# Optimization experiments

Measured on AMD Instinct MI355X. Metric: run time of the kernel, lower is better.

Reference implementation:

```python
import jax, jax.numpy as jnp
import numpy as np

DIM = 192
HEADS = 6
WS = 7          # window size
SHIFT = 3       # shift size
HID = 768       # mlp hidden
EPS = 1e-5


def _rel_pos_index(ws):
    coords = np.stack(np.meshgrid(np.arange(ws), np.arange(ws), indexing='ij'))  # (2, ws, ws)
    cf = coords.reshape(2, -1)                       # (2, ws*ws)
    rel = cf[:, :, None] - cf[:, None, :]            # (2, N, N)
    rel = rel.transpose(1, 2, 0).astype(np.int64)
    rel[:, :, 0] += ws - 1
    rel[:, :, 1] += ws - 1
    rel[:, :, 0] *= 2 * ws - 1
    return jnp.asarray(rel.sum(-1))                  # (N, N)

REL_IDX = _rel_pos_index(WS)


def _layernorm(x, w, b):
    mu = jnp.mean(x, axis=-1, keepdims=True)
    var = jnp.mean(jnp.square(x - mu), axis=-1, keepdims=True)
    return (x - mu) * jax.lax.rsqrt(var + EPS) * w + b


def setup_inputs() -> dict:
    key = jax.random.key(0)
    ks = jax.random.split(key, 8)
    B, H, W = 32, 56, 56
    s = 0.02
    return {
        'x': jax.random.normal(ks[0], (B, H * W, DIM), jnp.float32),
        'norm1_w': jnp.ones((DIM,), jnp.float32),
        'norm1_b': jnp.zeros((DIM,), jnp.float32),
        'qkv_w': jax.random.normal(ks[1], (3 * DIM, DIM), jnp.float32) * s,
        'qkv_b': jnp.zeros((3 * DIM,), jnp.float32),
        'rpb_table': jax.random.normal(ks[2], ((2 * WS - 1) ** 2, HEADS), jnp.float32) * s,
        'proj_w': jax.random.normal(ks[3], (DIM, DIM), jnp.float32) * s,
        'proj_b': jnp.zeros((DIM,), jnp.float32),
        'norm2_w': jnp.ones((DIM,), jnp.float32),
        'norm2_b': jnp.zeros((DIM,), jnp.float32),
        'fc1_w': jax.random.normal(ks[4], (HID, DIM), jnp.float32) * s,
        'fc1_b': jnp.zeros((HID,), jnp.float32),
        'fc2_w': jax.random.normal(ks[5], (DIM, HID), jnp.float32) * s,
        'fc2_b': jnp.zeros((DIM,), jnp.float32),
        'H': H,
        'W': W,
    }


def reference(x, norm1_w, norm1_b, qkv_w, qkv_b, rpb_table, proj_w, proj_b,
              norm2_w, norm2_b, fc1_w, fc1_b, fc2_w, fc2_b, H, W):
    B, L, C = x.shape
    d = C // HEADS
    scale = d ** -0.5
    N = WS * WS

    shortcut = x
    h = _layernorm(x, norm1_w, norm1_b).reshape(B, H, W, C)
    if SHIFT > 0:
        h = jnp.roll(h, shift=(-SHIFT, -SHIFT), axis=(1, 2))

    # window partition -> (B * nW, N, C)
    h = h.reshape(B, H // WS, WS, W // WS, WS, C).transpose(0, 1, 3, 2, 4, 5)
    hw = h.reshape(-1, N, C)

    # windowed attention (NOTE: the torch block never passes a shift mask)
    qkv = hw @ qkv_w.T + qkv_b                                    # (B_, N, 3C)
    qkv = qkv.reshape(-1, N, 3, HEADS, d).transpose(2, 0, 3, 1, 4)
    q, k, v = qkv[0] * scale, qkv[1], qkv[2]                      # (B_, h, N, d)
    attn = jnp.einsum('bhnd,bhmd->bhnm', q, k)
    bias = rpb_table[REL_IDX].transpose(2, 0, 1)                  # (h, N, N)
    attn = jax.nn.softmax(attn + bias[None], axis=-1)
    out = jnp.einsum('bhnm,bhmd->bhnd', attn, v)
    out = out.transpose(0, 2, 1, 3).reshape(-1, N, C)
    out = out @ proj_w.T + proj_b

    # window reverse -> (B, H, W, C)
    out = out.reshape(B, H // WS, W // WS, WS, WS, C).transpose(0, 1, 3, 2, 4, 5)
    out = out.reshape(B, H, W, C)
    if SHIFT > 0:
        out = jnp.roll(out, shift=(SHIFT, SHIFT), axis=(1, 2))

    x = shortcut + out.reshape(B, L, C)
    h2 = _layernorm(x, norm2_w, norm2_b)
    mlp = jax.nn.gelu(h2 @ fc1_w.T + fc1_b, approximate=False) @ fc2_w.T + fc2_b
    return x + mlp
```

## Files before the change

kernel.cpp:

```cpp
#include <hip/hip_runtime.h>
#include <hip/hip_bf16.h>
#include <cmath>

typedef float f32x4 __attribute__((ext_vector_type(4)));
typedef __bf16 bf16x8 __attribute__((ext_vector_type(8)));

#define WS_SZ 7
#define SHIFT 3
#define HGRID 56
#define C_DIM 192
#define NHEADS 6
#define HDIM 32
#define NTOK 100352
#define NWIN 2048

__device__ __forceinline__ int win_to_tok(int wrow) {
    int w = wrow / 49, i = wrow - w * 49;
    int b = w >> 6, rem = w & 63;
    int wy = rem >> 3, wx = rem & 7;
    int yi = i / 7, xi = i - yi * 7;
    int y = wy * 7 + yi + SHIFT; if (y >= HGRID) y -= HGRID;
    int x = wx * 7 + xi + SHIFT; if (x >= HGRID) x -= HGRID;
    return b * (HGRID * HGRID) + y * HGRID + x;
}

__global__ __launch_bounds__(256)
void cvt_kernel(const float* __restrict__ src, __bf16* __restrict__ dst, int n8)
{
    int idx = blockIdx.x * 256 + threadIdx.x;
    if (idx >= n8) return;
    float4 a = ((const float4*)src)[idx * 2];
    float4 b = ((const float4*)src)[idx * 2 + 1];
    bf16x8 o;
    o[0] = (__bf16)a.x; o[1] = (__bf16)a.y; o[2] = (__bf16)a.z; o[3] = (__bf16)a.w;
    o[4] = (__bf16)b.x; o[5] = (__bf16)b.y; o[6] = (__bf16)b.z; o[7] = (__bf16)b.w;
    ((bf16x8*)dst)[idx] = o;
}

__global__ __launch_bounds__(256)
void bias_expand_kernel(const float* __restrict__ rpb, float* __restrict__ bias_g)
{
    int idx = blockIdx.x * 256 + threadIdx.x;
    if (idx >= NHEADS * 2401) return;
    int h = idx / 2401, rem = idx - h * 2401;
    int i = rem / 49, j = rem - i * 49;
    int yi = i / 7, xi = i - yi * 7;
    int yj = j / 7, xj = j - yj * 7;
    int ri = (yi - yj + 6) * 13 + (xi - xj + 6);
    bias_g[idx] = rpb[ri * NHEADS + h];
}

template<int WINDOWED>
__global__ __launch_bounds__(256)
void ln_kernel(const float* __restrict__ x, const float* __restrict__ w,
               const float* __restrict__ b, __bf16* __restrict__ out)
{
    int r = blockIdx.x * 4 + (threadIdx.x >> 6);
    int lane = threadIdx.x & 63;
    int src = WINDOWED ? win_to_tok(r) : r;
    const float* xp = x + (size_t)src * C_DIM;
    float v0 = xp[lane], v1 = xp[lane + 64], v2 = xp[lane + 128];
    float s = v0 + v1 + v2;
    float sq = v0 * v0 + v1 * v1 + v2 * v2;
    #pragma unroll
    for (int off = 32; off; off >>= 1) {
        s  += __shfl_xor(s, off);
        sq += __shfl_xor(sq, off);
    }
    float mu = s * (1.f / C_DIM);
    float rs = rsqrtf(sq * (1.f / C_DIM) - mu * mu + 1e-5f);
    __bf16* op = out + (size_t)r * C_DIM;
    op[lane]       = (__bf16)((v0 - mu) * rs * w[lane]       + b[lane]);
    op[lane + 64]  = (__bf16)((v1 - mu) * rs * w[lane + 64]  + b[lane + 64]);
    op[lane + 128] = (__bf16)((v2 - mu) * rs * w[lane + 128] + b[lane + 128]);
}

template<int MODE>
__global__ __launch_bounds__(256)
void gemm_kernel(const __bf16* __restrict__ A, const __bf16* __restrict__ W,
                 const float* __restrict__ bias, void* __restrict__ outp,
                 const float* __restrict__ resid, int N, int K)
{
    __shared__ __bf16 As[128 * 40];
    __shared__ __bf16 Bs[64 * 40];
    const int tid = threadIdx.x;
    const int wave = tid >> 6, lane = tid & 63;
    const int wm = wave >> 1, wn = wave & 1;
    const int l15 = lane & 15, q8 = (lane >> 4) << 3;
    const int m0 = blockIdx.y * 128, n0 = blockIdx.x * 64;

    f32x4 acc[4][2];
    f32x4 zero = {0.f, 0.f, 0.f, 0.f};
    #pragma unroll
    for (int i = 0; i < 4; i++)
        #pragma unroll
        for (int j = 0; j < 2; j++) acc[i][j] = zero;

    const int br = tid >> 2, bc = (tid & 3) << 3;
    for (int kt = 0; kt < K; kt += 32) {
        __syncthreads();
        #pragma unroll
        for (int it = 0; it < 2; it++) {
            int idx = it * 256 + tid;
            int r = idx >> 2, c = (idx & 3) << 3;
            *(uint4*)(&As[r * 40 + c]) =
                *(const uint4*)(A + (size_t)(m0 + r) * K + kt + c);
        }
        *(uint4*)(&Bs[br * 40 + bc]) =
            *(const uint4*)(W + (size_t)(n0 + br) * K + kt + bc);
        __syncthreads();
        bf16x8 af[4], bfr[2];
        #pragma unroll
        for (int fm = 0; fm < 4; fm++)
            af[fm] = *(const bf16x8*)(&As[(wm * 64 + fm * 16 + l15) * 40 + q8]);
        #pragma unroll
        for (int fn = 0; fn < 2; fn++)
            bfr[fn] = *(const bf16x8*)(&Bs[(wn * 32 + fn * 16 + l15) * 40 + q8]);
        #pragma unroll
        for (int fm = 0; fm < 4; fm++)
            #pragma unroll
            for (int fn = 0; fn < 2; fn++)
                acc[fm][fn] = __builtin_amdgcn_mfma_f32_16x16x32_bf16(
                    af[fm], bfr[fn], acc[fm][fn], 0, 0, 0);
    }

    const int l4 = lane >> 4;
    #pragma unroll
    for (int fm = 0; fm < 4; fm++) {
        #pragma unroll
        for (int fn = 0; fn < 2; fn++) {
            int c = n0 + wn * 32 + fn * 16 + l15;
            float bv = bias[c];
            #pragma unroll
            for (int r = 0; r < 4; r++) {
                int m = m0 + wm * 64 + fm * 16 + l4 * 4 + r;
                float v = acc[fm][fn][r] + bv;
                if (MODE == 0) {
                    ((__bf16*)outp)[(size_t)m * N + c] = (__bf16)v;
                } else {
                    int t = win_to_tok(m);
                    ((float*)outp)[(size_t)t * C_DIM + c] =
                        resid[(size_t)t * C_DIM + c] + v;
                }
            }
        }
    }
}

__global__ __launch_bounds__(256, 3)
void mlp_fused_kernel(const float* __restrict__ n2w, const float* __restrict__ n2b,
                      const __bf16* __restrict__ w1,
                      const float* __restrict__ b1,
                      const __bf16* __restrict__ w2,
                      const float* __restrict__ b2,
                      float* __restrict__ out)
{
    __shared__ __bf16 As[64 * 200];
    __shared__ __bf16 Hs[64 * 136];
    const int tid = threadIdx.x;
    const int wn = tid >> 6, lane = tid & 63;
    const int l15 = lane & 15, q4 = lane >> 4, q8 = q4 << 3;
    const int m0 = blockIdx.x * 64;

    {
        const float wl0 = n2w[lane], wl1 = n2w[lane + 64], wl2 = n2w[lane + 128];
        const float bl0 = n2b[lane], bl1 = n2b[lane + 64], bl2 = n2b[lane + 128];
        const int r0 = wn * 16;
        for (int rr = 0; rr < 16; ++rr) {
            int r = r0 + rr;
            const float* xp = out + (size_t)(m0 + r) * C_DIM;
            float v0 = xp[lane], v1 = xp[lane + 64], v2 = xp[lane + 128];
            float s = v0 + v1 + v2;
            float sq = v0 * v0 + v1 * v1 + v2 * v2;
            #pragma unroll
            for (int off = 32; off; off >>= 1) {
                s  += __shfl_xor(s, off);
                sq += __shfl_xor(sq, off);
            }
            float mu = s * (1.f / C_DIM);
            float rs = rsqrtf(sq * (1.f / C_DIM) - mu * mu + 1e-5f);
            As[r * 200 + lane]       = (__bf16)((v0 - mu) * rs * wl0 + bl0);
            As[r * 200 + lane + 64]  = (__bf16)((v1 - mu) * rs * wl1 + bl1);
            As[r * 200 + lane + 128] = (__bf16)((v2 - mu) * rs * wl2 + bl2);
        }
    }
    __syncthreads();

    f32x4 zero = {0.f, 0.f, 0.f, 0.f};
    f32x4 acc2[4][3];
    #pragma unroll
    for (int tm = 0; tm < 4; ++tm)
        #pragma unroll
        for (int tn = 0; tn < 3; ++tn) acc2[tm][tn] = zero;

    for (int ch = 0; ch < 6; ++ch) {
        const int h0 = ch * 128;
        f32x4 acc1[4][2];
        #pragma unroll
        for (int tm = 0; tm < 4; ++tm)
            #pragma unroll
            for (int tn = 0; tn < 2; ++tn) acc1[tm][tn] = zero;
        #pragma unroll
        for (int kt = 0; kt < 6; ++kt) {
            bf16x8 bfr[2];
            #pragma unroll
            for (int tn = 0; tn < 2; ++tn)
                bfr[tn] = *(const bf16x8*)(w1 +
                    (size_t)(h0 + wn * 32 + tn * 16 + l15) * 192 + kt * 32 + q8);
            #pragma unroll
            for (int tm = 0; tm < 4; ++tm) {
                bf16x8 af = *(const bf16x8*)(&As[(tm * 16 + l15) * 200 + kt * 32 + q8]);
                #pragma unroll
                for (int tn = 0; tn < 2; ++tn)
                    acc1[tm][tn] = __builtin_amdgcn_mfma_f32_16x16x32_bf16(
                        af, bfr[tn], acc1[tm][tn], 0, 0, 0);
            }
        }
        __syncthreads();
        #pragma unroll
        for (int tm = 0; tm < 4; ++tm) {
            #pragma unroll
            for (int tn = 0; tn < 2; ++tn) {
                int col = wn * 32 + tn * 16 + l15;
                float bv = b1[h0 + col];
                #pragma unroll
                for (int r = 0; r < 4; ++r) {
                    int row = tm * 16 + q4 * 4 + r;
                    float v = acc1[tm][tn][r] + bv;
                    float e = __expf(-1.702f * v);
                    float g = v * __builtin_amdgcn_rcpf(1.f + e);
                    Hs[row * 136 + col] = (__bf16)g;
                }
            }
        }
        __syncthreads();
        #pragma unroll
        for (int ks = 0; ks < 4; ++ks) {
            bf16x8 bfr[3];
            #pragma unroll
            for (int tn = 0; tn < 3; ++tn)
                bfr[tn] = *(const bf16x8*)(w2 +
                    (size_t)(wn * 48 + tn * 16 + l15) * 768 + h0 + ks * 32 + q8);
            #pragma unroll
            for (int tm = 0; tm < 4; ++tm) {
                bf16x8 af = *(const bf16x8*)(&Hs[(tm * 16 + l15) * 136 + ks * 32 + q8]);
                #pragma unroll
                for (int tn = 0; tn < 3; ++tn)
                    acc2[tm][tn] = __builtin_amdgcn_mfma_f32_16x16x32_bf16(
                        af, bfr[tn], acc2[tm][tn], 0, 0, 0);
            }
        }
    }

    #pragma unroll
    for (int tm = 0; tm < 4; ++tm) {
        #pragma unroll
        for (int tn = 0; tn < 3; ++tn) {
            int c = wn * 48 + tn * 16 + l15;
            float bv = b2[c];
            #pragma unroll
            for (int r = 0; r < 4; ++r) {
                int m = m0 + tm * 16 + q4 * 4 + r;
                float* p = out + (size_t)m * C_DIM + c;
                *p = *p + acc2[tm][tn][r] + bv;
            }
        }
    }
}

__global__ __launch_bounds__(256, 2)
void attn_mfma_kernel(const __bf16* __restrict__ qkv,
                      const float* __restrict__ bias_g,
                      __bf16* __restrict__ out)
{
    const int wave = threadIdx.x >> 6;
    const int lane = threadIdx.x & 63;
    const int pair = blockIdx.x * 4 + wave;
    const int w = pair / 6, head = pair - (pair / 6) * 6;

    __shared__ __bf16 vsT_s[4][32 * 72];
    __shared__ __bf16 Ps_s[4][64 * 72];
    __bf16* vsT = vsT_s[wave];
    __bf16* Ps  = Ps_s[wave];

    const int l15 = lane & 15, q4 = lane >> 4, q8 = q4 << 3;
    const size_t qbase = (size_t)w * 49 * 576 + head * 32;

    {
        int d = lane & 31, jh = lane >> 5;
        #pragma unroll
        for (int it = 0; it < 25; ++it) {
            int j = it * 2 + jh;
            if (j < 49)
                vsT[d * 72 + j] = qkv[qbase + (size_t)j * 576 + 384 + d];
        }
        for (int idx = lane; idx < 32 * 15; idx += 64) {
            int dd = idx / 15, jj = 49 + (idx - dd * 15);
            vsT[dd * 72 + jj] = (__bf16)0.f;
        }
    }

    bf16x8 qf[4], kf[4];
    #pragma unroll
    for (int t = 0; t < 4; ++t) {
        int row = t * 16 + l15;
        int rq = row < 49 ? row : 48;
        qf[t] = *(const bf16x8*)(qkv + qbase + (size_t)rq * 576 + q8);
        kf[t] = *(const bf16x8*)(qkv + qbase + (size_t)rq * 576 + 192 + q8);
    }

    f32x4 sc[4][4];
    f32x4 zero = {0.f, 0.f, 0.f, 0.f};
    #pragma unroll
    for (int tm = 0; tm < 4; ++tm)
        #pragma unroll
        for (int tn = 0; tn < 4; ++tn) sc[tm][tn] = zero;
    #pragma unroll
    for (int tm = 0; tm < 4; ++tm)
        #pragma unroll
        for (int tn = 0; tn < 4; ++tn)
            sc[tm][tn] = __builtin_amdgcn_mfma_f32_16x16x32_bf16(
                qf[tm], kf[tn], sc[tm][tn], 0, 0, 0);

    const float scale = 0.17677669529663687f;
    const int hbase = head * 2401;
    #pragma unroll
    for (int tm = 0; tm < 4; ++tm) {
        #pragma unroll
        for (int r = 0; r < 4; ++r) {
            int i = tm * 16 + q4 * 4 + r;
            int ioff = hbase + (i < 49 ? i : 48) * 49;
            float v[4];
            #pragma unroll
            for (int tn = 0; tn < 4; ++tn) {
                int j = tn * 16 + l15;
                float bz = (j < 49) ? bias_g[ioff + (j < 49 ? j : 0)] : 0.f;
                float t = sc[tm][tn][r] * scale + bz;
                v[tn] = (j < 49) ? t : -1e30f;
            }
            float mx = fmaxf(fmaxf(v[0], v[1]), fmaxf(v[2], v[3]));
            mx = fmaxf(mx, __shfl_xor(mx, 1));
            mx = fmaxf(mx, __shfl_xor(mx, 2));
            mx = fmaxf(mx, __shfl_xor(mx, 4));
            mx = fmaxf(mx, __shfl_xor(mx, 8));
            float sm = 0.f;
            #pragma unroll
            for (int tn = 0; tn < 4; ++tn) {
                float e = __expf(v[tn] - mx);
                sc[tm][tn][r] = e;
                sm += e;
            }
            sm += __shfl_xor(sm, 1);
            sm += __shfl_xor(sm, 2);
            sm += __shfl_xor(sm, 4);
            sm += __shfl_xor(sm, 8);
            float inv = __builtin_amdgcn_rcpf(sm);
            if (i < 49) {
                #pragma unroll
                for (int tn = 0; tn < 4; ++tn) {
                    int j = tn * 16 + l15;
                    Ps[i * 72 + j] = (__bf16)((j < 49) ? sc[tm][tn][r] * inv : 0.f);
                }
            }
        }
    }

    __syncthreads();

    f32x4 oc[4][2];
    #pragma unroll
    for (int tm = 0; tm < 4; ++tm)
        #pragma unroll
        for (int tn = 0; tn < 2; ++tn) oc[tm][tn] = zero;
    #pragma unroll
    for (int ks = 0; ks < 2; ++ks) {
        bf16x8 bv[2];
        #pragma unroll
        for (int tn = 0; tn < 2; ++tn)
            bv[tn] = *(const bf16x8*)(vsT + (tn * 16 + l15) * 72 + ks * 32 + q8);
        #pragma unroll
        for (int tm = 0; tm < 4; ++tm) {
            bf16x8 ap = *(const bf16x8*)(Ps + (tm * 16 + l15) * 72 + ks * 32 + q8);
            #pragma unroll
            for (int tn = 0; tn < 2; ++tn)
                oc[tm][tn] = __builtin_amdgcn_mfma_f32_16x16x32_bf16(
                    ap, bv[tn], oc[tm][tn], 0, 0, 0);
        }
    }

    #pragma unroll
    for (int tm = 0; tm < 4; ++tm) {
        #pragma unroll
        for (int r = 0; r < 4; ++r) {
            int m = tm * 16 + q4 * 4 + r;
            if (m < 49) {
                __bf16* op = out + (size_t)(w * 49 + m) * C_DIM + head * 32;
                #pragma unroll
                for (int tn = 0; tn < 2; ++tn)
                    op[tn * 16 + l15] = (__bf16)(oc[tm][tn][r]);
            }
        }
    }
}

extern "C" void kernel_launch(void* const* d_in, const int* in_sizes, int n_in,
                              void* d_out, int out_size, void* d_ws, size_t ws_size,
                              hipStream_t stream) {
    const float* x     = (const float*)d_in[0];
    const float* n1w   = (const float*)d_in[1];
    const float* n1b   = (const float*)d_in[2];
    const float* qkvw  = (const float*)d_in[3];
    const float* qkvb  = (const float*)d_in[4];
    const float* rpb   = (const float*)d_in[5];
    const float* projw = (const float*)d_in[6];
    const float* projb = (const float*)d_in[7];
    const float* n2w   = (const float*)d_in[8];
    const float* n2b   = (const float*)d_in[9];
    const float* fc1w  = (const float*)d_in[10];
    const float* fc1b  = (const float*)d_in[11];
    const float* fc2w  = (const float*)d_in[12];
    const float* fc2b  = (const float*)d_in[13];
    float* out = (float*)d_out;
    char* ws = (char*)d_ws;

    __bf16* bufA    = (__bf16*)ws;
    __bf16* bufQ    = (__bf16*)(ws + 38535168);
    __bf16* qkvw_b  = (__bf16*)(ws + 154140672);
    __bf16* projw_b = (__bf16*)(ws + 154361856);
    __bf16* fc1w_b  = (__bf16*)(ws + 154435584);
    __bf16* fc2w_b  = (__bf16*)(ws + 154730496);
    float*  bias_g  = (float*) (ws + 155025408);

    cvt_kernel<<<(110592/8 + 255)/256, 256, 0, stream>>>(qkvw, qkvw_b, 110592/8);
    cvt_kernel<<<(36864/8  + 255)/256, 256, 0, stream>>>(projw, projw_b, 36864/8);
    cvt_kernel<<<(147456/8 + 255)/256, 256, 0, stream>>>(fc1w, fc1w_b, 147456/8);
    cvt_kernel<<<(147456/8 + 255)/256, 256, 0, stream>>>(fc2w, fc2w_b, 147456/8);
    bias_expand_kernel<<<(NHEADS*2401 + 255)/256, 256, 0, stream>>>(rpb, bias_g);

    ln_kernel<1><<<NTOK / 4, 256, 0, stream>>>(x, n1w, n1b, bufA);
    gemm_kernel<0><<<dim3(9, NTOK / 128), 256, 0, stream>>>(
        bufA, qkvw_b, qkvb, bufQ, nullptr, 576, 192);
    attn_mfma_kernel<<<NWIN * NHEADS / 4, 256, 0, stream>>>(bufQ, bias_g, bufA);
    gemm_kernel<1><<<dim3(3, NTOK / 128), 256, 0, stream>>>(
        bufA, projw_b, projb, (void*)out, x, 192, 192);
    mlp_fused_kernel<<<NTOK / 64, 256, 0, stream>>>(
        n2w, n2b, fc1w_b, fc1b, fc2w_b, fc2b, out);
}
```

Before: 510.9 us.

## Repartition fused MLP so each wave owns 16 rows and drops block barriers

The fused LN2+MLP kernel switches from splitting the N dimension across waves to giving each wave its own 16-row slice, with private LDS for the activations and the hidden chunk. This removes every __syncthreads in the kernel, and each wave now keeps one A fragment while looping over all N tiles. In exchange, every wave loads the full W1 and W2 tiles from global or cache, which is four times more weight traffic per block. The B-fragment arrays also grow (8 and 12 bf16x8), which raises register pressure. s_setprio is placed around the MFMA bursts.

```diff
diff --git a/kernel.cpp b/kernel.cpp
--- a/kernel.cpp
+++ b/kernel.cpp
@@ -156,19 +156,21 @@
                       float* __restrict__ out)
 {
     __shared__ __bf16 As[64 * 200];
-    __shared__ __bf16 Hs[64 * 136];
+    __shared__ __bf16 Hs[4][16 * 136];
     const int tid = threadIdx.x;
     const int wn = tid >> 6, lane = tid & 63;
     const int l15 = lane & 15, q4 = lane >> 4, q8 = q4 << 3;
     const int m0 = blockIdx.x * 64;
+    const int r0 = wn * 16;
+    __bf16* As_w = &As[r0 * 200];
+    __bf16* Hs_w = Hs[wn];
 
     {
         const float wl0 = n2w[lane], wl1 = n2w[lane + 64], wl2 = n2w[lane + 128];
         const float bl0 = n2b[lane], bl1 = n2b[lane + 64], bl2 = n2b[lane + 128];
-        const int r0 = wn * 16;
+        #pragma unroll
         for (int rr = 0; rr < 16; ++rr) {
-            int r = r0 + rr;
-            const float* xp = out + (size_t)(m0 + r) * C_DIM;
+            const float* xp = out + (size_t)(m0 + r0 + rr) * C_DIM;
             float v0 = xp[lane], v1 = xp[lane + 64], v2 = xp[lane + 128];
             float s = v0 + v1 + v2;
             float sq = v0 * v0 + v1 * v1 + v2 * v2;
@@ -179,91 +181,76 @@
             }
             float mu = s * (1.f / C_DIM);
             float rs = rsqrtf(sq * (1.f / C_DIM) - mu * mu + 1e-5f);
-            As[r * 200 + lane]       = (__bf16)((v0 - mu) * rs * wl0 + bl0);
-            As[r * 200 + lane + 64]  = (__bf16)((v1 - mu) * rs * wl1 + bl1);
-            As[r * 200 + lane + 128] = (__bf16)((v2 - mu) * rs * wl2 + bl2);
-        }
-    }
-    __syncthreads();
+            As_w[rr * 200 + lane]       = (__bf16)((v0 - mu) * rs * wl0 + bl0);
+            As_w[rr * 200 + lane + 64]  = (__bf16)((v1 - mu) * rs * wl1 + bl1);
+            As_w[rr * 200 + lane + 128] = (__bf16)((v2 - mu) * rs * wl2 + bl2);
+        }
+    }
 
     f32x4 zero = {0.f, 0.f, 0.f, 0.f};
-    f32x4 acc2[4][3];
-    #pragma unroll
-    for (int tm = 0; tm < 4; ++tm)
-        #pragma unroll
-        for (int tn = 0; tn < 3; ++tn) acc2[tm][tn] = zero;
+    f32x4 acc2[12];
+    #pragma unroll
+    for (int tn = 0; tn < 12; ++tn) acc2[tn] = zero;
 
     for (int ch = 0; ch < 6; ++ch) {
         const int h0 = ch * 128;
-        f32x4 acc1[4][2];
-        #pragma unroll
-        for (int tm = 0; tm < 4; ++tm)
-            #pragma unroll
-            for (int tn = 0; tn < 2; ++tn) acc1[tm][tn] = zero;
+        f32x4 acc1[8];
+        #pragma unroll
+        for (int tn = 0; tn < 8; ++tn) acc1[tn] = zero;
         #pragma unroll
         for (int kt = 0; kt < 6; ++kt) {
-            bf16x8 bfr[2];
-            #pragma unroll
-            for (int tn = 0; tn < 2; ++tn)
+            bf16x8 af = *(const bf16x8*)(&As_w[l15 * 200 + kt * 32 + q8]);
+            bf16x8 bfr[8];
+            #pragma unroll
+            for (int tn = 0; tn < 8; ++tn)
                 bfr[tn] = *(const bf16x8*)(w1 +
-                    (size_t)(h0 + wn * 32 + tn * 16 + l15) * 192 + kt * 32 + q8);
-            #pragma unroll
-            for (int tm = 0; tm < 4; ++tm) {
-                bf16x8 af = *(const bf16x8*)(&As[(tm * 16 + l15) * 200 + kt * 32 + q8]);
-                #pragma unroll
-                for (int tn = 0; tn < 2; ++tn)
-                    acc1[tm][tn] = __builtin_amdgcn_mfma_f32_16x16x32_bf16(
-                        af, bfr[tn], acc1[tm][tn], 0, 0, 0);
-            }
-        }
-        __syncthreads();
-        #pragma unroll
-        for (int tm = 0; tm < 4; ++tm) {
-            #pragma unroll
-            for (int tn = 0; tn < 2; ++tn) {
-                int col = wn * 32 + tn * 16 + l15;
-                float bv = b1[h0 + col];
-                #pragma unroll
-                for (int r = 0; r < 4; ++r) {
-                    int row = tm * 16 + q4 * 4 + r;
-                    float v = acc1[tm][tn][r] + bv;
-                    float e = __expf(-1.702f * v);
-                    float g = v * __builtin_amdgcn_rcpf(1.f + e);
-                    Hs[row * 136 + col] = (__bf16)g;
-                }
-            }
-        }
-        __syncthreads();
+                    (size_t)(h0 + tn * 16 + l15) * 192 + kt * 32 + q8);
+            __builtin_amdgcn_s_setprio(1);
+            #pragma unroll
+            for (int tn = 0; tn < 8; ++tn)
+                acc1[tn] = __builtin_amdgcn_mfma_f32_16x16x32_bf16(
+                    af, bfr[tn], acc1[tn], 0, 0, 0);
+            __builtin_amdgcn_s_setprio(0);
+        }
+        #pragma unroll
+        for (int tn = 0; tn < 8; ++tn) {
+            int col = tn * 16 + l15;
+            float bv = b1[h0 + col];
+            #pragma unroll
+            for (int r = 0; r < 4; ++r) {
+                int row = q4 * 4 + r;
+                float v = acc1[tn][r] + bv;
+                float e = __expf(-1.702f * v);
+                float g = v * __builtin_amdgcn_rcpf(1.f + e);
+                Hs_w[row * 136 + col] = (__bf16)g;
+            }
+        }
         #pragma unroll
         for (int ks = 0; ks < 4; ++ks) {
-            bf16x8 bfr[3];
-            #pragma unroll
-            for (int tn = 0; tn < 3; ++tn)
+            bf16x8 af = *(const bf16x8*)(&Hs_w[l15 * 136 + ks * 32 + q8]);
+            bf16x8 bfr[12];
+            #pragma unroll
+            for (int tn = 0; tn < 12; ++tn)
                 bfr[tn] = *(const bf16x8*)(w2 +
-                    (size_t)(wn * 48 + tn * 16 + l15) * 768 + h0 + ks * 32 + q8);
-            #pragma unroll
-            for (int tm = 0; tm < 4; ++tm) {
-                bf16x8 af = *(const bf16x8*)(&Hs[(tm * 16 + l15) * 136 + ks * 32 + q8]);
-                #pragma unroll
-                for (int tn = 0; tn < 3; ++tn)
-                    acc2[tm][tn] = __builtin_amdgcn_mfma_f32_16x16x32_bf16(
-                        af, bfr[tn], acc2[tm][tn], 0, 0, 0);
-            }
-        }
-    }
-
-    #pragma unroll
-    for (int tm = 0; tm < 4; ++tm) {
-        #pragma unroll
-        for (int tn = 0; tn < 3; ++tn) {
-            int c = wn * 48 + tn * 16 + l15;
-            float bv = b2[c];
-            #pragma unroll
-            for (int r = 0; r < 4; ++r) {
-                int m = m0 + tm * 16 + q4 * 4 + r;
-                float* p = out + (size_t)m * C_DIM + c;
-                *p = *p + acc2[tm][tn][r] + bv;
-            }
+                    (size_t)(tn * 16 + l15) * 768 + h0 + ks * 32 + q8);
+            __builtin_amdgcn_s_setprio(1);
+            #pragma unroll
+            for (int tn = 0; tn < 12; ++tn)
+                acc2[tn] = __builtin_amdgcn_mfma_f32_16x16x32_bf16(
+                    af, bfr[tn], acc2[tn], 0, 0, 0);
+            __builtin_amdgcn_s_setprio(0);
+        }
+    }
+
+    #pragma unroll
+    for (int tn = 0; tn < 12; ++tn) {
+        int c = tn * 16 + l15;
+        float bv = b2[c];
+        #pragma unroll
+        for (int r = 0; r < 4; ++r) {
+            int m = m0 + r0 + q4 * 4 + r;
+            float* p = out + (size_t)m * C_DIM + c;
+            *p = *p + acc2[tn][r] + bv;
         }
     }
 }
```

Result: slower. 821.6 us (+60.8%).

## Restructure fused MLP into 64-wide hidden chunks with register-prefetched weights

Applied to the files above, without the earlier changes.

The fused MLP kernel now walks the hidden dimension in twelve 64-wide chunks instead of six 128-wide ones, so each wave computes a single 16-column fc1 tile per chunk. The Hs staging buffer shrinks accordingly. fc1 weight fragments for the next chunk are double-buffered in registers and loaded ahead of use, the fc2 fragments are loaded at the top of each chunk, and the fc1 biases are preloaded once. The aim is to hide global-memory latency on the weight loads and cut LDS use, at the cost of more registers, full unrolling, and twice as many block-wide barriers.

```diff
diff --git a/kernel.cpp b/kernel.cpp
--- a/kernel.cpp
+++ b/kernel.cpp
@@ -156,19 +156,34 @@
                       float* __restrict__ out)
 {
     __shared__ __bf16 As[64 * 200];
-    __shared__ __bf16 Hs[64 * 136];
+    __shared__ __bf16 Hs[64 * 72];
     const int tid = threadIdx.x;
     const int wn = tid >> 6, lane = tid & 63;
     const int l15 = lane & 15, q4 = lane >> 4, q8 = q4 << 3;
     const int m0 = blockIdx.x * 64;
+    const int r0 = wn * 16;
+
+    const __bf16* w1base = w1 + (size_t)(wn * 16 + l15) * 192 + q8;
+    const __bf16* w2base = w2 + (size_t)(wn * 48 + l15) * 768 + q8;
+
+    f32x4 zero = {0.f, 0.f, 0.f, 0.f};
+
+    bf16x8 w1f[2][6];
+    #pragma unroll
+    for (int kt = 0; kt < 6; ++kt)
+        w1f[0][kt] = *(const bf16x8*)(w1base + kt * 32);
+
+    float bv1s[12];
+    #pragma unroll
+    for (int ch = 0; ch < 12; ++ch)
+        bv1s[ch] = b1[ch * 64 + wn * 16 + l15];
 
     {
         const float wl0 = n2w[lane], wl1 = n2w[lane + 64], wl2 = n2w[lane + 128];
         const float bl0 = n2b[lane], bl1 = n2b[lane + 64], bl2 = n2b[lane + 128];
-        const int r0 = wn * 16;
+        #pragma unroll
         for (int rr = 0; rr < 16; ++rr) {
-            int r = r0 + rr;
-            const float* xp = out + (size_t)(m0 + r) * C_DIM;
+            const float* xp = out + (size_t)(m0 + r0 + rr) * C_DIM;
             float v0 = xp[lane], v1 = xp[lane + 64], v2 = xp[lane + 128];
             float s = v0 + v1 + v2;
             float sq = v0 * v0 + v1 * v1 + v2 * v2;
@@ -179,77 +194,75 @@
             }
             float mu = s * (1.f / C_DIM);
             float rs = rsqrtf(sq * (1.f / C_DIM) - mu * mu + 1e-5f);
-            As[r * 200 + lane]       = (__bf16)((v0 - mu) * rs * wl0 + bl0);
-            As[r * 200 + lane + 64]  = (__bf16)((v1 - mu) * rs * wl1 + bl1);
-            As[r * 200 + lane + 128] = (__bf16)((v2 - mu) * rs * wl2 + bl2);
+            As[(r0 + rr) * 200 + lane]       = (__bf16)((v0 - mu) * rs * wl0 + bl0);
+            As[(r0 + rr) * 200 + lane + 64]  = (__bf16)((v1 - mu) * rs * wl1 + bl1);
+            As[(r0 + rr) * 200 + lane + 128] = (__bf16)((v2 - mu) * rs * wl2 + bl2);
         }
     }
     __syncthreads();
 
-    f32x4 zero = {0.f, 0.f, 0.f, 0.f};
     f32x4 acc2[4][3];
     #pragma unroll
     for (int tm = 0; tm < 4; ++tm)
         #pragma unroll
         for (int tn = 0; tn < 3; ++tn) acc2[tm][tn] = zero;
 
-    for (int ch = 0; ch < 6; ++ch) {
-        const int h0 = ch * 128;
-        f32x4 acc1[4][2];
-        #pragma unroll
-        for (int tm = 0; tm < 4; ++tm)
-            #pragma unroll
-            for (int tn = 0; tn < 2; ++tn) acc1[tm][tn] = zero;
-        #pragma unroll
-        for (int kt = 0; kt < 6; ++kt) {
-            bf16x8 bfr[2];
-            #pragma unroll
-            for (int tn = 0; tn < 2; ++tn)
-                bfr[tn] = *(const bf16x8*)(w1 +
-                    (size_t)(h0 + wn * 32 + tn * 16 + l15) * 192 + kt * 32 + q8);
+    bf16x8 w2f[6];
+
+    #pragma unroll
+    for (int ch = 0; ch < 12; ++ch) {
+        const int h0 = ch * 64;
+        const int cur = ch & 1, nxt = cur ^ 1;
+
+        if (ch < 11) {
+            #pragma unroll
+            for (int kt = 0; kt < 6; ++kt)
+                w1f[nxt][kt] = *(const bf16x8*)(w1base + (size_t)(h0 + 64) * 192 + kt * 32);
+        }
+        #pragma unroll
+        for (int ks = 0; ks < 2; ++ks)
+            #pragma unroll
+            for (int tn = 0; tn < 3; ++tn)
+                w2f[ks * 3 + tn] = *(const bf16x8*)(w2base + (size_t)(tn * 16) * 768 + h0 + ks * 32);
+
+        f32x4 acc1[4];
+        #pragma unroll
+        for (int tm = 0; tm < 4; ++tm) acc1[tm] = zero;
+        #pragma unroll
+        for (int kt = 0; kt < 6; ++kt)
             #pragma unroll
             for (int tm = 0; tm < 4; ++tm) {
                 bf16x8 af = *(const bf16x8*)(&As[(tm * 16 + l15) * 200 + kt * 32 + q8]);
-                #pragma unroll
-                for (int tn = 0; tn < 2; ++tn)
-                    acc1[tm][tn] = __builtin_amdgcn_mfma_f32_16x16x32_bf16(
-                        af, bfr[tn], acc1[tm][tn], 0, 0, 0);
-            }
-        }
+                acc1[tm] = __builtin_amdgcn_mfma_f32_16x16x32_bf16(
+                    af, w1f[cur][kt], acc1[tm], 0, 0, 0);
+            }
+
         __syncthreads();
-        #pragma unroll
-        for (int tm = 0; tm < 4; ++tm) {
-            #pragma unroll
-            for (int tn = 0; tn < 2; ++tn) {
-                int col = wn * 32 + tn * 16 + l15;
-                float bv = b1[h0 + col];
+
+        {
+            const float bv = bv1s[ch];
+            #pragma unroll
+            for (int tm = 0; tm < 4; ++tm)
                 #pragma unroll
                 for (int r = 0; r < 4; ++r) {
                     int row = tm * 16 + q4 * 4 + r;
-                    float v = acc1[tm][tn][r] + bv;
-                    float e = __expf(-1.702f * v);
-                    float g = v * __builtin_amdgcn_rcpf(1.f + e);
-                    Hs[row * 136 + col] = (__bf16)g;
+                    float v = acc1[tm][r] + bv;
+                    float g = v * __builtin_amdgcn_rcpf(1.f + __expf(-1.702f * v));
+                    Hs[row * 72 + wn * 16 + l15] = (__bf16)g;
                 }
-            }
         }
         __syncthreads();
-        #pragma unroll
-        for (int ks = 0; ks < 4; ++ks) {
-            bf16x8 bfr[3];
-            #pragma unroll
-            for (int tn = 0; tn < 3; ++tn)
-                bfr[tn] = *(const bf16x8*)(w2 +
-                    (size_t)(wn * 48 + tn * 16 + l15) * 768 + h0 + ks * 32 + q8);
+
+        #pragma unroll
+        for (int ks = 0; ks < 2; ++ks)
             #pragma unroll
             for (int tm = 0; tm < 4; ++tm) {
-                bf16x8 af = *(const bf16x8*)(&Hs[(tm * 16 + l15) * 136 + ks * 32 + q8]);
+                bf16x8 ap = *(const bf16x8*)(&Hs[(tm * 16 + l15) * 72 + ks * 32 + q8]);
                 #pragma unroll
                 for (int tn = 0; tn < 3; ++tn)
                     acc2[tm][tn] = __builtin_amdgcn_mfma_f32_16x16x32_bf16(
-                        af, bfr[tn], acc2[tm][tn], 0, 0, 0);
-            }
-        }
+                        ap, w2f[ks * 3 + tn], acc2[tm][tn], 0, 0, 0);
+            }
     }
 
     #pragma unroll
```

Result: faster. 481.8 us (-5.7%).
